# Kernel optimization log

Measured on AMD Instinct MI355X. Metric: run time of the kernel, lower is better.

Reference implementation:

```python
import jax, jax.numpy as jnp
import numpy as np

H, D = 4, 32            # heads, per-head out_channels (hidden_channels)
N, E = 50000, 800000    # nodes, edges
CIN, COUT = 256, 128    # conv in_channels, module out_channels


def setup_inputs() -> dict:
    key = jax.random.key(0)
    ks = jax.random.split(key, 20)
    w = lambda k, shape: (jax.random.normal(k, shape, jnp.float32) * 0.05)
    x = jax.random.normal(ks[0], (N, COUT), jnp.float32)
    t = jax.random.uniform(ks[1], (N, 1), dtype=jnp.float32)
    edge_index = jax.random.randint(ks[2], (2, E), 0, N)
    edge_weight = jax.random.uniform(ks[3], (E, 1), dtype=jnp.float32)
    return {
        'x': x, 't': t, 'edge_index': edge_index, 'edge_weight': edge_weight,
        # TransformerConv params (PyG): lin_query/key/value: Linear(CIN, H*D)
        'Wq': w(ks[4], (CIN, H * D)), 'bq': w(ks[5], (H * D,)),
        'Wk': w(ks[6], (CIN, H * D)), 'bk': w(ks[7], (H * D,)),
        'Wv': w(ks[8], (CIN, H * D)), 'bv': w(ks[9], (H * D,)),
        # lin_edge: Linear(edge_dim=1, H*D)
        'We': w(ks[10], (1, H * D)), 'be': w(ks[11], (H * D,)),
        # lin_skip (root weight, concat=False): Linear(CIN, D)
        'Wskip': w(ks[12], (CIN, D)), 'bskip': w(ks[13], (D,)),
        # mlp: Linear(D, 2*COUT) + tanh
        'Wmlp': w(ks[14], (D, 2 * COUT)), 'bmlp': w(ks[15], (2 * COUT,)),
    }


def _transformer_conv(y, edge_index, edge_attr, Wq, bq, Wk, bk, Wv, bv, We, be, Wskip, bskip):
    n = y.shape[0]
    q = (y @ Wq + bq).reshape(n, H, D)
    k = (y @ Wk + bk).reshape(n, H, D)
    v = (y @ Wv + bv).reshape(n, H, D)
    e = (edge_attr @ We + be).reshape(-1, H, D)          # [E,H,D]
    src, dst = edge_index[0], edge_index[1]
    k_e = k[src] + e                                     # edge-gathered keys
    alpha = jnp.einsum('ehd,ehd->eh', q[dst], k_e) / jnp.sqrt(jnp.float32(D))
    # segment softmax over incoming edges of each dst node
    m = jax.ops.segment_max(alpha, dst, num_segments=n)
    m = jnp.where(jnp.isfinite(m), m, 0.0)
    p = jnp.exp(alpha - m[dst])
    denom = jax.ops.segment_sum(p, dst, num_segments=n)
    attn = p / (denom[dst] + 1e-16)                      # [E,H]
    msg = (v[src] + e) * attn[..., None]                 # [E,H,D]
    agg = jax.ops.segment_sum(msg, dst, num_segments=n)  # [N,H,D]
    # concat=False -> mean over heads, plus root/skip term
    return agg.mean(axis=1) + y @ Wskip + bskip          # [N,D]


def reference(x, t, edge_index, edge_weight, Wq, bq, Wk, bk, Wv, bv, We, be, Wskip, bskip, Wmlp, bmlp):
    y0 = jnp.concatenate([x, x * t], axis=-1)            # [N, 2*COUT] = [N, CIN]
    y = _transformer_conv(y0, edge_index, edge_weight, Wq, bq, Wk, bk, Wv, bv, We, be, Wskip, bskip)
    y = jnp.tanh(y)                                      # activation after conv
    y = jnp.tanh(y @ Wmlp + bmlp)                        # mlp -> [N, 2*COUT]
    scale = y[:, :COUT]
    shift = y[:, COUT:]
    return x * scale + shift                             # FiLM conditioning (skip: identity x)
```

## Files before the change

### kernel.cpp

```cpp
#include <hip/hip_runtime.h>
#include <hip/hip_bf16.h>

#define NNODES 50000
#define NPAD   50048
#define NEDGES 800000
#define CAP 64
#define RSQRT_D 0.17677669529663687f

#define SCAT_BLOCKS 3125
#define GEMM_BLOCKS 1564

typedef short short8 __attribute__((ext_vector_type(8)));
typedef float f32x4 __attribute__((ext_vector_type(4)));

__device__ inline unsigned short f2bf(float f) {
    union { float f; unsigned u; } v; v.f = f;
    unsigned r = (v.u + 0x7fff + ((v.u >> 16) & 1)) >> 16;
    return (unsigned short)r;
}
__device__ inline float bf2f(unsigned short u) {
    union { unsigned u; float f; } v; v.u = ((unsigned)u) << 16;
    return v.f;
}
__device__ inline float bflo(unsigned u) {
    union { unsigned u; float f; } v; v.u = u << 16; return v.f;
}
__device__ inline float bfhi(unsigned u) {
    union { unsigned u; float f; } v; v.u = u & 0xffff0000u; return v.f;
}
__device__ inline float fast_tanh(float v) {
    const float e = __expf(2.0f * v);
    return 1.0f - 2.0f * __builtin_amdgcn_rcpf(e + 1.0f);
}

__global__ __launch_bounds__(256) void prep_w(
    const float* __restrict__ Wq, const float* __restrict__ bq,
    const float* __restrict__ Wk, const float* __restrict__ bk,
    const float* __restrict__ Wv, const float* __restrict__ bv,
    const float* __restrict__ Wskip, const float* __restrict__ bskip,
    unsigned short* __restrict__ Wtf, float* __restrict__ biascat)
{
    const int col = blockIdx.x;
    const int k = threadIdx.x;
    float v; float b;
    if (col < 128)      { v = Wq[k * 128 + col];          b = bq[col]; }
    else if (col < 256) { v = Wk[k * 128 + col - 128];    b = bk[col - 128]; }
    else if (col < 384) { v = Wv[k * 128 + col - 256];    b = bv[col - 256]; }
    else                { v = Wskip[k * 32 + col - 384];  b = bskip[col - 384]; }
    const int ct = col >> 4, c16 = col & 15;
    const int kt = k >> 5, quad = (k >> 3) & 3, j = k & 7;
    Wtf[(size_t)(ct * 32 + kt * 4 + quad) * 128 + c16 * 8 + j] = f2bf(v);
    if (k == 0) biascat[col] = b;
}

__global__ __launch_bounds__(256) void pack_a(
    const float* __restrict__ x, const float* __restrict__ t,
    unsigned short* __restrict__ y0f)
{
    const int gid = blockIdx.x * 256 + threadIdx.x;
    const int row = gid >> 5;
    const int oct = gid & 31;
    short8 out = {0, 0, 0, 0, 0, 0, 0, 0};
    if (row < NNODES) {
        const int kb = oct * 8;
        const int kx = (kb < 128) ? kb : (kb - 128);
        const float* xr = x + (size_t)row * 128 + kx;
        float4 f0 = *(const float4*)xr;
        float4 f1 = *(const float4*)(xr + 4);
        if (kb >= 128) {
            const float tv = t[row];
            f0.x *= tv; f0.y *= tv; f0.z *= tv; f0.w *= tv;
            f1.x *= tv; f1.y *= tv; f1.z *= tv; f1.w *= tv;
        }
        out[0] = (short)f2bf(f0.x); out[1] = (short)f2bf(f0.y);
        out[2] = (short)f2bf(f0.z); out[3] = (short)f2bf(f0.w);
        out[4] = (short)f2bf(f1.x); out[5] = (short)f2bf(f1.y);
        out[6] = (short)f2bf(f1.z); out[7] = (short)f2bf(f1.w);
    }
    *(short8*)(y0f + (size_t)((row >> 4) * 32 + oct) * 128 + (row & 15) * 8) = out;
}

#define LOADW(buf, ct) do {                                                    \
    _Pragma("unroll")                                                          \
    for (int kt_ = 0; kt_ < 8; ++kt_)                                          \
        buf[kt_] = *(const short8*)(Wtf + (size_t)((ct) * 32 + kt_ * 4 + quad) * 128 + l16 * 8); \
} while (0)

#define DOTILE(buf, ct) do {                                                   \
    f32x4 acc0 = {0.f, 0.f, 0.f, 0.f}, acc1 = {0.f, 0.f, 0.f, 0.f};            \
    _Pragma("unroll")                                                          \
    for (int kt_ = 0; kt_ < 8; ++kt_) {                                        \
        acc0 = __builtin_amdgcn_mfma_f32_16x16x32_bf16(buf[kt_], b0[kt_], acc0, 0, 0, 0); \
        acc1 = __builtin_amdgcn_mfma_f32_16x16x32_bf16(buf[kt_], b1[kt_], acc1, 0, 0, 0); \
    }                                                                          \
    const int cb_ = (ct) * 16 + quad * 4;                                      \
    const float4 bias_ = *(const float4*)(biascat + cb_);                      \
    _Pragma("unroll")                                                          \
    for (int s_ = 0; s_ < 2; ++s_) {                                           \
        const int m_ = n0 + s_ * 16 + l16;                                     \
        if (m_ < NNODES) {                                                     \
            const f32x4 a_ = s_ ? acc1 : acc0;                                 \
            const float v0_ = a_[0] + bias_.x, v1_ = a_[1] + bias_.y;          \
            const float v2_ = a_[2] + bias_.z, v3_ = a_[3] + bias_.w;          \
            if ((ct) < 24) {                                                   \
                uint2 pk_;                                                     \
                pk_.x = (unsigned)f2bf(v0_) | ((unsigned)f2bf(v1_) << 16);     \
                pk_.y = (unsigned)f2bf(v2_) | ((unsigned)f2bf(v3_) << 16);     \
                if ((ct) < 8)                                                  \
                    *(uint2*)(Qb + (size_t)m_ * 128 + cb_) = pk_;              \
                else                                                           \
                    *(uint2*)(KVb + (size_t)m_ * 256 + (cb_ - 128)) = pk_;     \
            } else {                                                           \
                *(float4*)(S + (size_t)m_ * 32 + (cb_ - 384)) =                \
                    make_float4(v0_, v1_, v2_, v3_);                           \
            }                                                                  \
        }                                                                      \
    }                                                                          \
} while (0)

__global__ __launch_bounds__(256) void gemm_scatter(
    const unsigned short* __restrict__ y0f,
    const unsigned short* __restrict__ Wtf,
    const float* __restrict__ biascat,
    unsigned short* __restrict__ Qb, unsigned short* __restrict__ KVb,
    float* __restrict__ S,
    const int* __restrict__ ei, const float* __restrict__ ew,
    int* __restrict__ cnt, int2* __restrict__ einfo)
{
    const int b = blockIdx.x;
    const int group = b / 3;
    const int r = b - group * 3;

    if (r < 2) {
        const int sb = group * 2 + r;
        if (sb >= SCAT_BLOCKS) return;
        const int e = sb * 256 + threadIdx.x;
        const int src = ei[e];
        const int dst = ei[NEDGES + e];
        const int pos = atomicAdd(&cnt[dst], 1);
        if (pos < CAP) {
            int2 v; v.x = src; v.y = __float_as_int(ew[e]);
            einfo[(size_t)dst * CAP + pos] = v;
        }
        return;
    }

    const int g = group;
    const int bx = g % 391;
    const int by = g / 391;

    const int tid = threadIdx.x;
    const int wave = tid >> 6;
    const int lane = tid & 63;
    const int l16 = lane & 15;
    const int quad = lane >> 4;

    const int n0 = bx * 128 + wave * 32;
    const int mt0 = n0 >> 4;
    const int ct0 = by * 7 - ((by >= 2) ? (by - 2) : 0);
    const int nct = (by < 2) ? 7 : 6;
    const int ctEnd = ct0 + nct;

    short8 b0[8], b1[8];
    #pragma unroll
    for (int kt = 0; kt < 8; ++kt) {
        b0[kt] = *(const short8*)(y0f + (size_t)((mt0 + 0) * 32 + kt * 4 + quad) * 128 + l16 * 8);
        b1[kt] = *(const short8*)(y0f + (size_t)((mt0 + 1) * 32 + kt * 4 + quad) * 128 + l16 * 8);
    }

    short8 wa[8], wb[8];
    LOADW(wa, ct0);
    for (int ct = ct0; ct < ctEnd; ct += 2) {
        if (ct + 1 < ctEnd) LOADW(wb, ct + 1);
        DOTILE(wa, ct);
        if (ct + 1 < ctEnd) {
            if (ct + 2 < ctEnd) LOADW(wa, ct + 2);
            DOTILE(wb, ct + 1);
        }
    }
}

__global__ __launch_bounds__(256) void agg_pass(
    const int* __restrict__ cnt, const int2* __restrict__ einfo,
    const float* __restrict__ We, const float* __restrict__ be,
    const unsigned short* __restrict__ Qb, const unsigned short* __restrict__ KVb,
    float* __restrict__ G)
{
    const int tid = threadIdx.x;
    const int node = blockIdx.x * 4 + (tid >> 6);
    if (node >= NNODES) return;
    const int l = tid & 63;
    const int slot = l >> 4;
    const int q = l & 15;

    const uint4 qu = *(const uint4*)(Qb + (size_t)node * 128 + q * 8);
    float qv[8];
    qv[0] = bflo(qu.x); qv[1] = bfhi(qu.x);
    qv[2] = bflo(qu.y); qv[3] = bfhi(qu.y);
    qv[4] = bflo(qu.z); qv[5] = bfhi(qu.z);
    qv[6] = bflo(qu.w); qv[7] = bfhi(qu.w);

    const float4 weA = *(const float4*)(We + q * 8);
    const float4 weB = *(const float4*)(We + q * 8 + 4);
    const float4 beA = *(const float4*)(be + q * 8);
    const float4 beB = *(const float4*)(be + q * 8 + 4);

    float pw = qv[0]*weA.x + qv[1]*weA.y + qv[2]*weA.z + qv[3]*weA.w
             + qv[4]*weB.x + qv[5]*weB.y + qv[6]*weB.z + qv[7]*weB.w;
    float pb = qv[0]*beA.x + qv[1]*beA.y + qv[2]*beA.z + qv[3]*beA.w
             + qv[4]*beB.x + qv[5]*beB.y + qv[6]*beB.z + qv[7]*beB.w;
    pw += __shfl_xor(pw, 1); pb += __shfl_xor(pb, 1);
    pw += __shfl_xor(pw, 2); pb += __shfl_xor(pb, 2);
    const float qWeS = pw * RSQRT_D;
    const float qbeS = pb * RSQRT_D;

    const int deg = min(cnt[node], CAP);
    const int2* ep = einfo + (size_t)node * CAP;

    int2 eall = make_int2(0, 0);
    const int loadN = min(CAP, ((deg + 3) & ~3) + 4);
    if (l < loadN) eall = ep[l];

    float a[8] = {0.f, 0.f, 0.f, 0.f, 0.f, 0.f, 0.f, 0.f};
    float sp = 0.f, spw = 0.f;

    const char* kvb = (const char*)KVb;
    const unsigned qoff = (unsigned)(q * 16);

    int ecx = __shfl(eall.x, slot);
    int ecy = __shfl(eall.y, slot);
    bool vc = (slot < deg);
    {
        const unsigned off = (((unsigned)(vc ? ecx : 0)) << 9) + qoff;
        uint4 kw = *(const uint4*)(kvb + off);
        uint4 vw = *(const uint4*)(kvb + off + 256);
        float wc = __int_as_float(ecy);

        for (int jj = 0; jj < deg; jj += 4) {
            const int nidx = (jj + 4 + slot) & 63;
            const int enx = __shfl(eall.x, nidx);
            const int eny = __shfl(eall.y, nidx);
            const bool vn = (jj + 4 + slot < deg);
            const unsigned offn = (((unsigned)(vn ? enx : 0)) << 9) + qoff;
            const uint4 kwn = *(const uint4*)(kvb + offn);
            const uint4 vwn = *(const uint4*)(kvb + offn + 256);
            const float wn = __int_as_float(eny);

            float d = qv[0]*bflo(kw.x) + qv[1]*bfhi(kw.x)
                    + qv[2]*bflo(kw.y) + qv[3]*bfhi(kw.y)
                    + qv[4]*bflo(kw.z) + qv[5]*bfhi(kw.z)
                    + qv[6]*bflo(kw.w) + qv[7]*bfhi(kw.w);
            d += __shfl_xor(d, 1);
            d += __shfl_xor(d, 2);
            float p = __expf(d * RSQRT_D + wc * qWeS + qbeS);
            p = vc ? p : 0.f;
            sp += p; spw += p * wc;
            a[0] += p * bflo(vw.x); a[1] += p * bfhi(vw.x);
            a[2] += p * bflo(vw.y); a[3] += p * bfhi(vw.y);
            a[4] += p * bflo(vw.z); a[5] += p * bfhi(vw.z);
            a[6] += p * bflo(vw.w); a[7] += p * bfhi(vw.w);

            kw = kwn; vw = vwn; wc = wn; vc = vn;
        }
    }

    sp  += __shfl_xor(sp, 16);  sp  += __shfl_xor(sp, 32);
    spw += __shfl_xor(spw, 16); spw += __shfl_xor(spw, 32);
    #pragma unroll
    for (int i = 0; i < 8; ++i) {
        a[i] += __shfl_xor(a[i], 16);
        a[i] += __shfl_xor(a[i], 32);
    }

    const float inv = 1.f / (sp + 1e-16f);
    a[0] = (a[0] + spw*weA.x + sp*beA.x) * inv;
    a[1] = (a[1] + spw*weA.y + sp*beA.y) * inv;
    a[2] = (a[2] + spw*weA.z + sp*beA.z) * inv;
    a[3] = (a[3] + spw*weA.w + sp*beA.w) * inv;
    a[4] = (a[4] + spw*weB.x + sp*beB.x) * inv;
    a[5] = (a[5] + spw*weB.y + sp*beB.y) * inv;
    a[6] = (a[6] + spw*weB.z + sp*beB.z) * inv;
    a[7] = (a[7] + spw*weB.w + sp*beB.w) * inv;

    #pragma unroll
    for (int i = 0; i < 8; ++i) {
        a[i] += __shfl_xor(a[i], 4);
        a[i] += __shfl_xor(a[i], 8);
    }

    if (l < 4) {
        *(float4*)(G + (size_t)node * 32 + q * 8) =
            make_float4(a[0]*0.25f, a[1]*0.25f, a[2]*0.25f, a[3]*0.25f);
        *(float4*)(G + (size_t)node * 32 + q * 8 + 4) =
            make_float4(a[4]*0.25f, a[5]*0.25f, a[6]*0.25f, a[7]*0.25f);
    }
}

__global__ __launch_bounds__(256, 4) void node_pass(
    const float* __restrict__ x,
    const float* __restrict__ G, const float* __restrict__ S,
    const float* __restrict__ Wmlp, const float* __restrict__ bmlp,
    float* __restrict__ out)
{
    __shared__ float yl[64 * 32];

    const int tid = threadIdx.x;
    const int c = tid & 127;
    const int half = tid >> 7;

    float w1[32], w2[32];
    #pragma unroll
    for (int d = 0; d < 32; ++d) {
        w1[d] = Wmlp[d * 256 + c];
        w2[d] = Wmlp[d * 256 + c + 128];
    }
    const float b1 = bmlp[c];
    const float b2 = bmlp[c + 128];

    const int n0 = blockIdx.x * 64;

    for (int i4 = tid; i4 < 512; i4 += 256) {
        const int n = n0 + (i4 >> 3);
        const int d0 = (i4 & 7) * 4;
        float4 yv = make_float4(0.f, 0.f, 0.f, 0.f);
        if (n < NNODES) {
            const float4 gv = *(const float4*)(G + (size_t)n * 32 + d0);
            const float4 sv = *(const float4*)(S + (size_t)n * 32 + d0);
            yv.x = fast_tanh(gv.x + sv.x);
            yv.y = fast_tanh(gv.y + sv.y);
            yv.z = fast_tanh(gv.z + sv.z);
            yv.w = fast_tanh(gv.w + sv.w);
        }
        *(float4*)&yl[i4 * 4] = yv;
    }
    __syncthreads();

    for (int k = 0; k < 32; ++k) {
        const int nl = 2 * k + half;
        const int n = n0 + nl;
        if (n >= NNODES) continue;

        const float4* yr = (const float4*)&yl[nl * 32];
        float s1 = b1, s2 = b2;
        #pragma unroll
        for (int d8 = 0; d8 < 8; ++d8) {
            const float4 y4 = yr[d8];
            s1 = fmaf(y4.x, w1[d8 * 4 + 0], s1);
            s2 = fmaf(y4.x, w2[d8 * 4 + 0], s2);
            s1 = fmaf(y4.y, w1[d8 * 4 + 1], s1);
            s2 = fmaf(y4.y, w2[d8 * 4 + 1], s2);
            s1 = fmaf(y4.z, w1[d8 * 4 + 2], s1);
            s2 = fmaf(y4.z, w2[d8 * 4 + 2], s2);
            s1 = fmaf(y4.w, w1[d8 * 4 + 3], s1);
            s2 = fmaf(y4.w, w2[d8 * 4 + 3], s2);
        }
        const float z1 = fast_tanh(s1);
        const float z2 = fast_tanh(s2);
        out[(size_t)n * 128 + c] = fmaf(x[(size_t)n * 128 + c], z1, z2);
    }
}

extern "C" void kernel_launch(void* const* d_in, const int* in_sizes, int n_in,
                              void* d_out, int out_size, void* d_ws, size_t ws_size,
                              hipStream_t stream) {
    const float* x     = (const float*)d_in[0];
    const float* t     = (const float*)d_in[1];
    const int*   ei    = (const int*)  d_in[2];
    const float* ew    = (const float*)d_in[3];
    const float* Wq    = (const float*)d_in[4];
    const float* bq    = (const float*)d_in[5];
    const float* Wk    = (const float*)d_in[6];
    const float* bk    = (const float*)d_in[7];
    const float* Wv    = (const float*)d_in[8];
    const float* bv    = (const float*)d_in[9];
    const float* We    = (const float*)d_in[10];
    const float* be    = (const float*)d_in[11];
    const float* Wskip = (const float*)d_in[12];
    const float* bskip = (const float*)d_in[13];
    const float* Wmlp  = (const float*)d_in[14];
    const float* bmlp  = (const float*)d_in[15];

    char* p = (char*)d_ws;
    unsigned short* Qb  = (unsigned short*)p; p += (size_t)NNODES * 128 * 2;
    unsigned short* KVb = (unsigned short*)p; p += (size_t)NNODES * 256 * 2;
    float* S       = (float*)p; p += (size_t)NNODES * 32 * 4;
    float* G       = (float*)p; p += (size_t)NNODES * 32 * 4;
    unsigned short* Wtf = (unsigned short*)p; p += 416 * 256 * 2;
    float* biascat = (float*)p; p += 416 * 4;
    unsigned short* y0f = (unsigned short*)p; p += (size_t)NPAD * 256 * 2;
    int2* einfo    = (int2*)p;  p += (size_t)NNODES * CAP * 8;
    int* cnt       = (int*)p;   p += NNODES * 4;

    hipMemsetAsync(cnt, 0, (size_t)NNODES * sizeof(int), stream);

    prep_w<<<416, 256, 0, stream>>>(Wq, bq, Wk, bk, Wv, bv, Wskip, bskip,
                                    Wtf, biascat);

    pack_a<<<(NPAD * 32) / 256, 256, 0, stream>>>(x, t, y0f);

    gemm_scatter<<<GEMM_BLOCKS * 3, 256, 0, stream>>>(
        y0f, Wtf, biascat, Qb, KVb, S, ei, ew, cnt, einfo);

    agg_pass<<<(NNODES + 3) / 4, 256, 0, stream>>>(cnt, einfo, We, be, Qb, KVb, G);

    node_pass<<<(NNODES + 63) / 64, 256, 0, stream>>>(x, G, S, Wmlp, bmlp,
                                                      (float*)d_out);
}
```

Before: 246.8 us.

## Fuse prep kernels and memset; fold edge scatter into GEMM blocks

The zeroing of the edge counters, the weight repack and the input pack now run as one launch instead of a memset plus two kernels. The edge scatter no longer uses its own dedicated blocks: each GEMM thread now handles two edges. It loads their indices up front, issues the atomics after the activation loads, and writes the edge records after the first MFMA tile. This removes launch overhead and tries to hide atomic and scatter latency behind matrix work. The cost is higher register pressure and a longer serial path in each GEMM block.

```diff
diff --git a/kernel.cpp b/kernel.cpp
--- a/kernel.cpp
+++ b/kernel.cpp
@@ -7,8 +7,12 @@
 #define CAP 64
 #define RSQRT_D 0.17677669529663687f
 
-#define SCAT_BLOCKS 3125
 #define GEMM_BLOCKS 1564
+#define EHALF 400384
+
+#define PACKA_BLOCKS 6256
+#define PREPW_BLOCKS 416
+#define CNT_BLOCKS   196
 
 typedef short short8 __attribute__((ext_vector_type(8)));
 typedef float f32x4 __attribute__((ext_vector_type(4)));
@@ -33,51 +37,59 @@
     return 1.0f - 2.0f * __builtin_amdgcn_rcpf(e + 1.0f);
 }
 
-__global__ __launch_bounds__(256) void prep_w(
+__global__ __launch_bounds__(256) void prep_pack(
     const float* __restrict__ Wq, const float* __restrict__ bq,
     const float* __restrict__ Wk, const float* __restrict__ bk,
     const float* __restrict__ Wv, const float* __restrict__ bv,
     const float* __restrict__ Wskip, const float* __restrict__ bskip,
-    unsigned short* __restrict__ Wtf, float* __restrict__ biascat)
+    const float* __restrict__ x, const float* __restrict__ t,
+    unsigned short* __restrict__ Wtf, float* __restrict__ biascat,
+    unsigned short* __restrict__ y0f, int* __restrict__ cnt)
 {
-    const int col = blockIdx.x;
-    const int k = threadIdx.x;
-    float v; float b;
-    if (col < 128)      { v = Wq[k * 128 + col];          b = bq[col]; }
-    else if (col < 256) { v = Wk[k * 128 + col - 128];    b = bk[col - 128]; }
-    else if (col < 384) { v = Wv[k * 128 + col - 256];    b = bv[col - 256]; }
-    else                { v = Wskip[k * 32 + col - 384];  b = bskip[col - 384]; }
-    const int ct = col >> 4, c16 = col & 15;
-    const int kt = k >> 5, quad = (k >> 3) & 3, j = k & 7;
-    Wtf[(size_t)(ct * 32 + kt * 4 + quad) * 128 + c16 * 8 + j] = f2bf(v);
-    if (k == 0) biascat[col] = b;
-}
-
-__global__ __launch_bounds__(256) void pack_a(
-    const float* __restrict__ x, const float* __restrict__ t,
-    unsigned short* __restrict__ y0f)
-{
-    const int gid = blockIdx.x * 256 + threadIdx.x;
-    const int row = gid >> 5;
-    const int oct = gid & 31;
-    short8 out = {0, 0, 0, 0, 0, 0, 0, 0};
-    if (row < NNODES) {
-        const int kb = oct * 8;
-        const int kx = (kb < 128) ? kb : (kb - 128);
-        const float* xr = x + (size_t)row * 128 + kx;
-        float4 f0 = *(const float4*)xr;
-        float4 f1 = *(const float4*)(xr + 4);
-        if (kb >= 128) {
-            const float tv = t[row];
-            f0.x *= tv; f0.y *= tv; f0.z *= tv; f0.w *= tv;
-            f1.x *= tv; f1.y *= tv; f1.z *= tv; f1.w *= tv;
+    const int b = blockIdx.x;
+    const int tid = threadIdx.x;
+
+    if (b < PACKA_BLOCKS) {
+        const int gid = b * 256 + tid;
+        const int row = gid >> 5;
+        const int oct = gid & 31;
+        short8 out = {0, 0, 0, 0, 0, 0, 0, 0};
+        if (row < NNODES) {
+            const int kb = oct * 8;
+            const int kx = (kb < 128) ? kb : (kb - 128);
+            const float* xr = x + (size_t)row * 128 + kx;
+            float4 f0 = *(const float4*)xr;
+            float4 f1 = *(const float4*)(xr + 4);
+            if (kb >= 128) {
+                const float tv = t[row];
+                f0.x *= tv; f0.y *= tv; f0.z *= tv; f0.w *= tv;
+                f1.x *= tv; f1.y *= tv; f1.z *= tv; f1.w *= tv;
+            }
+            out[0] = (short)f2bf(f0.x); out[1] = (short)f2bf(f0.y);
+            out[2] = (short)f2bf(f0.z); out[3] = (short)f2bf(f0.w);
+            out[4] = (short)f2bf(f1.x); out[5] = (short)f2bf(f1.y);
+            out[6] = (short)f2bf(f1.z); out[7] = (short)f2bf(f1.w);
         }
-        out[0] = (short)f2bf(f0.x); out[1] = (short)f2bf(f0.y);
-        out[2] = (short)f2bf(f0.z); out[3] = (short)f2bf(f0.w);
-        out[4] = (short)f2bf(f1.x); out[5] = (short)f2bf(f1.y);
-        out[6] = (short)f2bf(f1.z); out[7] = (short)f2bf(f1.w);
-    }
-    *(short8*)(y0f + (size_t)((row >> 4) * 32 + oct) * 128 + (row & 15) * 8) = out;
+        *(short8*)(y0f + (size_t)((row >> 4) * 32 + oct) * 128 + (row & 15) * 8) = out;
+        return;
+    }
+    const int b2 = b - PACKA_BLOCKS;
+    if (b2 < PREPW_BLOCKS) {
+        const int col = b2;
+        const int k = tid;
+        float v; float bb;
+        if (col < 128)      { v = Wq[k * 128 + col];          bb = bq[col]; }
+        else if (col < 256) { v = Wk[k * 128 + col - 128];    bb = bk[col - 128]; }
+        else if (col < 384) { v = Wv[k * 128 + col - 256];    bb = bv[col - 256]; }
+        else                { v = Wskip[k * 32 + col - 384];  bb = bskip[col - 384]; }
+        const int ct = col >> 4, c16 = col & 15;
+        const int kt = k >> 5, quad = (k >> 3) & 3, j = k & 7;
+        Wtf[(size_t)(ct * 32 + kt * 4 + quad) * 128 + c16 * 8 + j] = f2bf(v);
+        if (k == 0) biascat[col] = bb;
+        return;
+    }
+    const int idx = (b2 - PREPW_BLOCKS) * 256 + tid;
+    if (idx < NNODES) cnt[idx] = 0;
 }
 
 #define LOADW(buf, ct) do {                                                    \
@@ -127,29 +139,21 @@
     const int* __restrict__ ei, const float* __restrict__ ew,
     int* __restrict__ cnt, int2* __restrict__ einfo)
 {
-    const int b = blockIdx.x;
-    const int group = b / 3;
-    const int r = b - group * 3;
-
-    if (r < 2) {
-        const int sb = group * 2 + r;
-        if (sb >= SCAT_BLOCKS) return;
-        const int e = sb * 256 + threadIdx.x;
-        const int src = ei[e];
-        const int dst = ei[NEDGES + e];
-        const int pos = atomicAdd(&cnt[dst], 1);
-        if (pos < CAP) {
-            int2 v; v.x = src; v.y = __float_as_int(ew[e]);
-            einfo[(size_t)dst * CAP + pos] = v;
-        }
-        return;
-    }
-
-    const int g = group;
+    const int g = blockIdx.x;
+    const int tid = threadIdx.x;
+
+    const int gid = g * 256 + tid;
+    const int e0 = gid;
+    const int e1 = gid + EHALF;
+    const bool m1 = e1 < NEDGES;
+    const int  s0 = ei[e0];
+    const int  d0 = ei[NEDGES + e0];
+    const float w0 = ew[e0];
+    int s1 = 0, d1 = 0; float w1 = 0.f;
+    if (m1) { s1 = ei[e1]; d1 = ei[NEDGES + e1]; w1 = ew[e1]; }
+
     const int bx = g % 391;
     const int by = g / 391;
-
-    const int tid = threadIdx.x;
     const int wave = tid >> 6;
     const int lane = tid & 63;
     const int l16 = lane & 15;
@@ -168,14 +172,29 @@
         b1[kt] = *(const short8*)(y0f + (size_t)((mt0 + 1) * 32 + kt * 4 + quad) * 128 + l16 * 8);
     }
 
+    const int pos0 = atomicAdd(&cnt[d0], 1);
+    const int pos1 = m1 ? atomicAdd(&cnt[d1], 1) : CAP;
+
     short8 wa[8], wb[8];
     LOADW(wa, ct0);
-    for (int ct = ct0; ct < ctEnd; ct += 2) {
-        if (ct + 1 < ctEnd) LOADW(wb, ct + 1);
-        DOTILE(wa, ct);
+    LOADW(wb, ct0 + 1);
+    DOTILE(wa, ct0);
+
+    if (pos0 < CAP) {
+        int2 v; v.x = s0; v.y = __float_as_int(w0);
+        einfo[(size_t)d0 * CAP + pos0] = v;
+    }
+    if (pos1 < CAP) {
+        int2 v; v.x = s1; v.y = __float_as_int(w1);
+        einfo[(size_t)d1 * CAP + pos1] = v;
+    }
+
+    for (int ct = ct0 + 1; ct < ctEnd; ct += 2) {
+        if (ct + 1 < ctEnd) LOADW(wa, ct + 1);
+        DOTILE(wb, ct);
         if (ct + 1 < ctEnd) {
-            if (ct + 2 < ctEnd) LOADW(wa, ct + 2);
-            DOTILE(wb, ct + 1);
+            if (ct + 2 < ctEnd) LOADW(wb, ct + 2);
+            DOTILE(wa, ct + 1);
         }
     }
 }
@@ -391,14 +410,10 @@
     int2* einfo    = (int2*)p;  p += (size_t)NNODES * CAP * 8;
     int* cnt       = (int*)p;   p += NNODES * 4;
 
-    hipMemsetAsync(cnt, 0, (size_t)NNODES * sizeof(int), stream);
-
-    prep_w<<<416, 256, 0, stream>>>(Wq, bq, Wk, bk, Wv, bv, Wskip, bskip,
-                                    Wtf, biascat);
-
-    pack_a<<<(NPAD * 32) / 256, 256, 0, stream>>>(x, t, y0f);
-
-    gemm_scatter<<<GEMM_BLOCKS * 3, 256, 0, stream>>>(
+    prep_pack<<<PACKA_BLOCKS + PREPW_BLOCKS + CNT_BLOCKS, 256, 0, stream>>>(
+        Wq, bq, Wk, bk, Wv, bv, Wskip, bskip, x, t, Wtf, biascat, y0f, cnt);
+
+    gemm_scatter<<<GEMM_BLOCKS, 256, 0, stream>>>(
         y0f, Wtf, biascat, Qb, KVb, S, ei, ew, cnt, einfo);
 
     agg_pass<<<(NNODES + 3) / 4, 256, 0, stream>>>(cnt, einfo, We, be, Qb, KVb, G);
```

New measurement: 256.0 us. 3.7% more time.
